# Optimization experiments

Measured on AMD Instinct MI355X. Metric: run time of the kernel, lower is better.

## Reference

```python
import jax, jax.numpy as jnp
import numpy as np


def _soft_attention(h, context, W_in, W_out):
    """Luong soft-dot attention. h: [B,H], context: [B,L,H].
    W_in: [H,H] (in,out layout), W_out: [2H,H]."""
    target = h @ W_in                                  # [B, H]
    attn = jnp.einsum('blh,bh->bl', context, target)   # [B, L]
    p = jax.nn.softmax(attn, axis=-1)                  # [B, L]
    weighted_ctx = jnp.einsum('bl,blh->bh', p, context)  # [B, H]
    h_tilde = jnp.tanh(jnp.concatenate([weighted_ctx, h], axis=1) @ W_out)  # [B, H]
    return h_tilde, p


def setup_inputs() -> dict:
    key = jax.random.key(0)
    ks = jax.random.split(key, 13)
    B, L, H = 64, 512, 1024
    s2 = 1.0 / np.sqrt(2 * H)
    s1 = 1.0 / np.sqrt(H)
    return {
        'h_tilde_s': jax.random.normal(ks[0], (B, H), jnp.float32),
        'h_tilde_o': jax.random.normal(ks[1], (B, H), jnp.float32),
        'h_tilde_a': jax.random.normal(ks[2], (B, H), jnp.float32),
        'enc_out': jax.random.normal(ks[3], (B, L, H), jnp.float32),
        'full_feature_len': 36,
        'W_as': jax.random.normal(ks[4], (2 * H, H), jnp.float32) * s2,
        'W_so': jax.random.normal(ks[5], (2 * H, H), jnp.float32) * s2,
        'W_oa': jax.random.normal(ks[6], (2 * H, H), jnp.float32) * s2,
        'Win_as': jax.random.normal(ks[7], (H, H), jnp.float32) * s1,
        'Win_so': jax.random.normal(ks[8], (H, H), jnp.float32) * s1,
        'Win_oa': jax.random.normal(ks[9], (H, H), jnp.float32) * s1,
        'Wout_as': jax.random.normal(ks[10], (2 * H, H), jnp.float32) * s2,
        'Wout_so': jax.random.normal(ks[11], (2 * H, H), jnp.float32) * s2,
        'Wout_oa': jax.random.normal(ks[12], (2 * H, H), jnp.float32) * s2,
    }


def reference(h_tilde_s, h_tilde_o, h_tilde_a, enc_out, full_feature_len,
              W_as, W_so, W_oa, Win_as, Win_so, Win_oa,
              Wout_as, Wout_so, Wout_oa):
    # Relational contexts via concat + linear(no bias) + tanh
    h_as = jnp.tanh(jnp.concatenate([h_tilde_a, h_tilde_s], axis=1) @ W_as)  # [B,H]
    h_so = jnp.tanh(jnp.concatenate([h_tilde_s, h_tilde_o], axis=1) @ W_so)
    h_oa = jnp.tanh(jnp.concatenate([h_tilde_o, h_tilde_a], axis=1) @ W_oa)
    # Three parallel soft-dot attentions over encoder output
    sa_as, _ = _soft_attention(h_as, enc_out, Win_as, Wout_as)
    sa_so, _ = _soft_attention(h_so, enc_out, Win_so, Wout_so)
    sa_oa, _ = _soft_attention(h_oa, enc_out, Win_oa, Wout_oa)
    B, H = sa_as.shape
    F = full_feature_len
    # repeat_interleave of size-1 dim == broadcast tile to [B, F, H]
    ctx_mas = jnp.broadcast_to(sa_as[:, None, :], (B, F, H))
    ctx_mso = jnp.broadcast_to(sa_so[:, None, :], (B, F, H))
    ctx_moa = jnp.broadcast_to(sa_oa[:, None, :], (B, F, H))
    return (ctx_mas, ctx_mso, ctx_moa)
```

## Files before the change

kernel.cpp:

```cpp
#include <hip/hip_runtime.h>
#include <hip/hip_cooperative_groups.h>

namespace cg = cooperative_groups;

constexpr int BB = 64;
constexpr int LL = 512;
constexpr int HH = 1024;
constexpr int SPLITS = 16;
constexpr int GRID  = 512;
constexpr int NTHR  = 256;
constexpr int NWORK_GEMM = 3 * 16 * SPLITS;

typedef float nt_float4 __attribute__((ext_vector_type(4)));

struct Args {
    const float* hs; const float* ho; const float* ha; const float* enc;
    const int* Fp;
    const float* W_as;  const float* W_so;  const float* W_oa;
    const float* Win_as; const float* Win_so; const float* Win_oa;
    const float* Wout_as; const float* Wout_so; const float* Wout_oa;
    float* part; float* hx; float* tt; float* wc; float* opm; float* ms;
    float* out;
};

template<int K0, int K1>
__device__ __forceinline__ void gemm_tile(const float* __restrict__ a0,
                                          const float* __restrict__ a1,
                                          const float* __restrict__ w,
                                          float* __restrict__ part_r,
                                          int nt, int sp, int tid,
                                          float (*As)[64], float (*Ws)[64])
{
    constexpr int K = K0 + K1;
    constexpr int KRANGE = K / SPLITS;
    const int n0 = nt << 6;
    const int ks = sp * KRANGE;
    const int tn = tid & 15;
    const int tm = tid >> 4;

    float acc[4][4] = {};

    for (int kt = ks; kt < ks + KRANGE; kt += 32) {
        {
            const int m   = tid >> 2;
            const int kk0 = (tid & 3) << 3;
            const int kg  = kt + kk0;
            const float* src = (K1 == 0 || kg < K0) ? (a0 + (size_t)m * HH + kg)
                                                    : (a1 + (size_t)m * HH + (kg - K0));
            float4 v0 = *(const float4*)(src);
            float4 v1 = *(const float4*)(src + 4);
            As[kk0 + 0][m] = v0.x; As[kk0 + 1][m] = v0.y;
            As[kk0 + 2][m] = v0.z; As[kk0 + 3][m] = v0.w;
            As[kk0 + 4][m] = v1.x; As[kk0 + 5][m] = v1.y;
            As[kk0 + 6][m] = v1.z; As[kk0 + 7][m] = v1.w;
        }
        {
            const int j4 = (tid & 15) << 2;
            int kk = tid >> 4;
            #pragma unroll
            for (int i = 0; i < 2; i++, kk += 16) {
                *(float4*)&Ws[kk][j4] = *(const float4*)(w + (size_t)(kt + kk) * HH + n0 + j4);
            }
        }
        __syncthreads();
        #pragma unroll
        for (int kk = 0; kk < 32; kk++) {
            float4 a4 = *(const float4*)&As[kk][tm << 2];
            float4 b4 = *(const float4*)&Ws[kk][tn << 2];
            float av[4] = {a4.x, a4.y, a4.z, a4.w};
            float bv[4] = {b4.x, b4.y, b4.z, b4.w};
            #pragma unroll
            for (int i = 0; i < 4; i++)
                #pragma unroll
                for (int j = 0; j < 4; j++)
                    acc[i][j] += av[i] * bv[j];
        }
        __syncthreads();
    }

    float* dst = part_r + (size_t)(sp << 6) * HH + n0 + (tn << 2);
    #pragma unroll
    for (int i = 0; i < 4; i++) {
        const int m = (tm << 2) + i;
        *(float4*)(dst + (size_t)m * HH) = make_float4(acc[i][0], acc[i][1], acc[i][2], acc[i][3]);
    }
}

__device__ __forceinline__ void gemmA_work(const Args& a, int wk, int tid,
                                           float (*As)[64], float (*Ws)[64])
{
    const int r  = wk >> 8;
    const int nt = wk & 15;
    const int sp = (wk >> 4) & 15;
    const float* a0 = (r == 0) ? a.ha : (r == 1) ? a.hs : a.ho;
    const float* a1 = (r == 0) ? a.hs : (r == 1) ? a.ho : a.ha;
    const float* w  = (r == 0) ? a.W_as : (r == 1) ? a.W_so : a.W_oa;
    gemm_tile<1024, 1024>(a0, a1, w, a.part + (size_t)r * SPLITS * 65536,
                          nt, sp, tid, As, Ws);
}

__device__ __forceinline__ void gemmC_work(const Args& a, int wk, int tid,
                                           float (*As)[64], float (*Ws)[64])
{
    const int r  = wk >> 8;
    const int nt = wk & 15;
    const int sp = (wk >> 4) & 15;
    const float* a0 = a.hx + (size_t)r * 65536;
    const float* w  = (r == 0) ? a.Win_as : (r == 1) ? a.Win_so : a.Win_oa;
    gemm_tile<1024, 0>(a0, nullptr, w, a.part + (size_t)r * SPLITS * 65536,
                       nt, sp, tid, As, Ws);
}

__device__ __forceinline__ void gemmG_work(const Args& a, int wk, int tid,
                                           float (*As)[64], float (*Ws)[64])
{
    const int r  = wk >> 8;
    const int nt = wk & 15;
    const int sp = (wk >> 4) & 15;
    const float* a0 = a.wc + (size_t)r * 65536;
    const float* a1 = a.hx + (size_t)r * 65536;
    const float* w  = (r == 0) ? a.Wout_as : (r == 1) ? a.Wout_so : a.Wout_oa;
    gemm_tile<1024, 1024>(a0, a1, w, a.part + (size_t)r * SPLITS * 65536,
                          nt, sp, tid, As, Ws);
}

__device__ __forceinline__ void reduce_phase(const float* __restrict__ part,
                                             float* __restrict__ dst,
                                             int gtid, bool do_tanh)
{
    if (gtid >= 49152) return;
    const int flat = gtid << 2;
    const int r    = flat >> 16;
    const int mn   = flat & 65535;
    const float* p = part + (size_t)r * SPLITS * 65536 + mn;
    float4 s = *(const float4*)p;
    #pragma unroll
    for (int y = 1; y < SPLITS; y++) {
        float4 q = *(const float4*)(p + (size_t)y * 65536);
        s.x += q.x; s.y += q.y; s.z += q.z; s.w += q.w;
    }
    if (do_tanh) {
        s.x = tanhf(s.x); s.y = tanhf(s.y); s.z = tanhf(s.z); s.w = tanhf(s.w);
    }
    *(float4*)(dst + (size_t)r * 65536 + mn) = s;
}

__device__ __forceinline__ void flash_phase(const Args& args, int chunk, int tid,
                                            float* smem)
{
    float (*o_l)[HH]     = (float(*)[HH])smem;
    float (*ms_sh)[3][2] = (float(*)[3][2])(smem + 4096);
    const int b    = chunk >> 3;
    const int lc   = chunk & 7;
    const int lane = tid & 63;
    const int wv   = tid >> 6;

    float4 tr[3][4];
    #pragma unroll
    for (int r = 0; r < 3; r++)
        #pragma unroll
        for (int v = 0; v < 4; v++)
            tr[r][v] = *(const float4*)&args.tt[(size_t)(r * BB + b) * HH + (lane << 2) + (v << 8)];

    float  m_run[3] = {-3.0e38f, -3.0e38f, -3.0e38f};
    float  S_run[3] = {0.f, 0.f, 0.f};
    float4 o_run[3][4];
    #pragma unroll
    for (int r = 0; r < 3; r++)
        #pragma unroll
        for (int v = 0; v < 4; v++)
            o_run[r][v] = make_float4(0.f, 0.f, 0.f, 0.f);

    const float* ebase = args.enc + ((size_t)b * LL + (lc << 6) + (wv << 2)) * HH + (lane << 2);

    for (int it = 0; it < 4; it++) {
        const float* e = ebase + (size_t)(it << 4) * HH;
        float4 ev[4][4];
        #pragma unroll
        for (int j = 0; j < 4; j++)
            #pragma unroll
            for (int v = 0; v < 4; v++)
                ev[j][v] = *(const float4*)(e + (size_t)j * HH + (v << 8));

        float s[3][4];
        #pragma unroll
        for (int j = 0; j < 4; j++) {
            float d0 = 0.f, d1 = 0.f, d2 = 0.f;
            #pragma unroll
            for (int v = 0; v < 4; v++) {
                const float4 x = ev[j][v];
                d0 += x.x * tr[0][v].x + x.y * tr[0][v].y + x.z * tr[0][v].z + x.w * tr[0][v].w;
                d1 += x.x * tr[1][v].x + x.y * tr[1][v].y + x.z * tr[1][v].z + x.w * tr[1][v].w;
                d2 += x.x * tr[2][v].x + x.y * tr[2][v].y + x.z * tr[2][v].z + x.w * tr[2][v].w;
            }
            #pragma unroll
            for (int off = 32; off > 0; off >>= 1) {
                d0 += __shfl_xor(d0, off);
                d1 += __shfl_xor(d1, off);
                d2 += __shfl_xor(d2, off);
            }
            s[0][j] = d0; s[1][j] = d1; s[2][j] = d2;
        }

        #pragma unroll
        for (int r = 0; r < 3; r++) {
            const float mb = fmaxf(fmaxf(s[r][0], s[r][1]), fmaxf(s[r][2], s[r][3]));
            const float mn_ = fmaxf(m_run[r], mb);
            const float alpha = __expf(m_run[r] - mn_);
            m_run[r] = mn_;
            float p[4];
            float psum = 0.f;
            #pragma unroll
            for (int j = 0; j < 4; j++) { p[j] = __expf(s[r][j] - mn_); psum += p[j]; }
            S_run[r] = S_run[r] * alpha + psum;
            #pragma unroll
            for (int v = 0; v < 4; v++) {
                float4 o = o_run[r][v];
                o.x *= alpha; o.y *= alpha; o.z *= alpha; o.w *= alpha;
                #pragma unroll
                for (int j = 0; j < 4; j++) {
                    const float4 x = ev[j][v];
                    o.x += p[j] * x.x; o.y += p[j] * x.y;
                    o.z += p[j] * x.z; o.w += p[j] * x.w;
                }
                o_run[r][v] = o;
            }
        }
    }

    if (lane == 0) {
        #pragma unroll
        for (int r = 0; r < 3; r++) { ms_sh[wv][r][0] = m_run[r]; ms_sh[wv][r][1] = S_run[r]; }
    }

    #pragma unroll
    for (int r = 0; r < 3; r++) {
        __syncthreads();
        #pragma unroll
        for (int v = 0; v < 4; v++)
            *(float4*)&o_l[wv][(lane << 2) + (v << 8)] = o_run[r][v];
        __syncthreads();

        const float m0 = ms_sh[0][r][0], m1 = ms_sh[1][r][0];
        const float m2 = ms_sh[2][r][0], m3 = ms_sh[3][r][0];
        const float M = fmaxf(fmaxf(m0, m1), fmaxf(m2, m3));
        const float w0 = __expf(m0 - M), w1 = __expf(m1 - M);
        const float w2 = __expf(m2 - M), w3 = __expf(m3 - M);
        float4 q0 = *(const float4*)&o_l[0][tid << 2];
        float4 q1 = *(const float4*)&o_l[1][tid << 2];
        float4 q2 = *(const float4*)&o_l[2][tid << 2];
        float4 q3 = *(const float4*)&o_l[3][tid << 2];
        float4 acc;
        acc.x = w0 * q0.x + w1 * q1.x + w2 * q2.x + w3 * q3.x;
        acc.y = w0 * q0.y + w1 * q1.y + w2 * q2.y + w3 * q3.y;
        acc.z = w0 * q0.z + w1 * q1.z + w2 * q2.z + w3 * q3.z;
        acc.w = w0 * q0.w + w1 * q1.w + w2 * q2.w + w3 * q3.w;
        *(float4*)&args.opm[((size_t)chunk * 3 + r) * HH + (tid << 2)] = acc;
        if (tid == 0) {
            const float S = w0 * ms_sh[0][r][1] + w1 * ms_sh[1][r][1]
                          + w2 * ms_sh[2][r][1] + w3 * ms_sh[3][r][1];
            args.ms[((size_t)chunk * 3 + r) * 2 + 0] = M;
            args.ms[((size_t)chunk * 3 + r) * 2 + 1] = S;
        }
    }
}

__device__ __forceinline__ void combine_phase(const Args& args, int b, int r, int tid)
{
    float mv[8], sv[8];
    float M = -3.0e38f;
    #pragma unroll
    for (int c = 0; c < 8; c++) {
        const int chunk = (b << 3) + c;
        mv[c] = args.ms[((size_t)chunk * 3 + r) * 2 + 0];
        sv[c] = args.ms[((size_t)chunk * 3 + r) * 2 + 1];
        M = fmaxf(M, mv[c]);
    }
    float S = 0.f;
    float4 acc = make_float4(0.f, 0.f, 0.f, 0.f);
    #pragma unroll
    for (int c = 0; c < 8; c++) {
        const float wgt = __expf(mv[c] - M);
        S += wgt * sv[c];
        const int chunk = (b << 3) + c;
        float4 q = *(const float4*)&args.opm[((size_t)chunk * 3 + r) * HH + (tid << 2)];
        acc.x += wgt * q.x; acc.y += wgt * q.y;
        acc.z += wgt * q.z; acc.w += wgt * q.w;
    }
    const float inv = 1.0f / S;
    acc.x *= inv; acc.y *= inv; acc.z *= inv; acc.w *= inv;
    *(float4*)&args.wc[(size_t)(r * BB + b) * HH + (tid << 2)] = acc;
}

__device__ __forceinline__ void broadcast_phase(const Args& args, int gtid)
{
    const int flat = gtid << 2;
    const int r    = flat >> 16;
    const int mn   = flat & 65535;
    const float* p = args.part + (size_t)r * SPLITS * 65536 + mn;
    float4 s = *(const float4*)p;
    #pragma unroll
    for (int y = 1; y < SPLITS; y++) {
        float4 q = *(const float4*)(p + (size_t)y * 65536);
        s.x += q.x; s.y += q.y; s.z += q.z; s.w += q.w;
    }
    s.x = tanhf(s.x); s.y = tanhf(s.y); s.z = tanhf(s.z); s.w = tanhf(s.w);

    nt_float4 sv;
    sv.x = s.x; sv.y = s.y; sv.z = s.z; sv.w = s.w;

    const int F  = *args.Fp;
    const int bb = mn >> 10;
    const int hh = mn & 1023;
    float* o = args.out + ((size_t)(r * BB + bb) * F) * HH + hh;
    for (int f = 0; f < F; f++)
        __builtin_nontemporal_store(sv, (nt_float4*)(o + (size_t)f * HH));
}

__global__ __launch_bounds__(NTHR, 2)
void mega_kernel(Args args)
{
    __shared__ __align__(16) float smem[4224];
    cg::grid_group grid = cg::this_grid();
    const int bid  = blockIdx.x;
    const int tid  = threadIdx.x;
    const int gtid = bid * NTHR + tid;

    float (*As)[64] = (float(*)[64])smem;
    float (*Ws)[64] = (float(*)[64])(smem + 2048);

    for (int wk = bid; wk < NWORK_GEMM; wk += gridDim.x)
        gemmA_work(args, wk, tid, As, Ws);
    grid.sync();

    reduce_phase(args.part, args.hx, gtid, true);
    grid.sync();

    for (int wk = bid; wk < NWORK_GEMM; wk += gridDim.x)
        gemmC_work(args, wk, tid, As, Ws);
    grid.sync();

    reduce_phase(args.part, args.tt, gtid, false);
    grid.sync();

    flash_phase(args, bid, tid, smem);
    grid.sync();

    if (bid < 192)
        combine_phase(args, bid & 63, bid >> 6, tid);
    grid.sync();

    for (int wk = bid; wk < NWORK_GEMM; wk += gridDim.x)
        gemmG_work(args, wk, tid, As, Ws);
    grid.sync();

    if (gtid < 49152)
        broadcast_phase(args, gtid);
}

__global__ __launch_bounds__(NTHR)
void k_gemmA(Args a)
{
    __shared__ __align__(16) float smem[4096];
    gemmA_work(a, blockIdx.x, threadIdx.x, (float(*)[64])smem, (float(*)[64])(smem + 2048));
}

__global__ __launch_bounds__(NTHR)
void k_gemmC(Args a)
{
    __shared__ __align__(16) float smem[4096];
    gemmC_work(a, blockIdx.x, threadIdx.x, (float(*)[64])smem, (float(*)[64])(smem + 2048));
}

__global__ __launch_bounds__(NTHR)
void k_gemmG(Args a)
{
    __shared__ __align__(16) float smem[4096];
    gemmG_work(a, blockIdx.x, threadIdx.x, (float(*)[64])smem, (float(*)[64])(smem + 2048));
}

__global__ __launch_bounds__(NTHR)
void k_reduceB(Args a) { reduce_phase(a.part, a.hx, blockIdx.x * NTHR + threadIdx.x, true); }

__global__ __launch_bounds__(NTHR)
void k_reduceD(Args a) { reduce_phase(a.part, a.tt, blockIdx.x * NTHR + threadIdx.x, false); }

__global__ __launch_bounds__(NTHR)
void k_flash(Args a)
{
    __shared__ __align__(16) float smem[4224];
    flash_phase(a, blockIdx.x, threadIdx.x, smem);
}

__global__ __launch_bounds__(NTHR)
void k_combine(Args a) { combine_phase(a, blockIdx.x, blockIdx.y, threadIdx.x); }

__global__ __launch_bounds__(NTHR)
void k_broadcast(Args a)
{
    const int gtid = blockIdx.x * NTHR + threadIdx.x;
    if (gtid < 49152) broadcast_phase(a, gtid);
}

extern "C" void kernel_launch(void* const* d_in, const int* in_sizes, int n_in,
                              void* d_out, int out_size, void* d_ws, size_t ws_size,
                              hipStream_t stream)
{
    (void)in_sizes; (void)n_in; (void)out_size; (void)ws_size;
    float* ws = (float*)d_ws;

    Args a;
    a.hs  = (const float*)d_in[0];
    a.ho  = (const float*)d_in[1];
    a.ha  = (const float*)d_in[2];
    a.enc = (const float*)d_in[3];
    a.Fp  = (const int*)d_in[4];
    a.W_as    = (const float*)d_in[5];
    a.W_so    = (const float*)d_in[6];
    a.W_oa    = (const float*)d_in[7];
    a.Win_as  = (const float*)d_in[8];
    a.Win_so  = (const float*)d_in[9];
    a.Win_oa  = (const float*)d_in[10];
    a.Wout_as = (const float*)d_in[11];
    a.Wout_so = (const float*)d_in[12];
    a.Wout_oa = (const float*)d_in[13];

    a.part = ws;
    a.hx   = ws + 3145728;
    a.tt   = ws + 3342336;
    a.wc   = ws + 3538944;
    a.opm  = ws + 3735552;
    a.ms   = ws + 5308416;
    a.out  = (float*)d_out;

    static int coop = -2;
    if (coop == -2) {
        int dev = 0, cus = 0, nb = 0;
        hipGetDevice(&dev);
        hipDeviceGetAttribute(&cus, hipDeviceAttributeMultiprocessorCount, dev);
        hipError_t e = hipOccupancyMaxActiveBlocksPerMultiprocessor(&nb, mega_kernel, NTHR, 0);
        coop = (e == hipSuccess && nb > 0 && (long)nb * cus >= GRID) ? 1 : 0;
    }

    bool launched = false;
    if (coop == 1) {
        void* kargs[] = { (void*)&a };
        hipError_t e = hipLaunchCooperativeKernel((const void*)mega_kernel,
                                                  dim3(GRID), dim3(NTHR),
                                                  kargs, 0, stream);
        launched = (e == hipSuccess);
        if (!launched) coop = 0;
    }

    if (!launched) {
        k_gemmA<<<NWORK_GEMM, NTHR, 0, stream>>>(a);
        k_reduceB<<<192, NTHR, 0, stream>>>(a);
        k_gemmC<<<NWORK_GEMM, NTHR, 0, stream>>>(a);
        k_reduceD<<<192, NTHR, 0, stream>>>(a);
        k_flash<<<512, NTHR, 0, stream>>>(a);
        k_combine<<<dim3(64, 3), NTHR, 0, stream>>>(a);
        k_gemmG<<<NWORK_GEMM, NTHR, 0, stream>>>(a);
        k_broadcast<<<192, NTHR, 0, stream>>>(a);
    }
}
```

Measured before the change: 327.4 us.

## Size cooperative grid to occupancy, split flash chunks finer, prefetch GEMM tiles

Lets the cooperative mega-kernel grid scale to occupancy (up to 1024 blocks, launch bounds raised to 4 blocks per CU) and converts every phase to grid-stride loops. The flash-attention phase is split into 1024 chunks of 32 rows each, so combine merges 16 partials per batch row; the opm/ms workspace offsets are adjusted to fit. The GEMM tile loop now register-prefetches the next A/W slice while computing the current one. Together these aim to fill more CUs and hide global latency, at the cost of more register pressure and more combine work.

Result: slower. 822.0 us (+151.1%).

```diff
diff --git a/kernel.cpp b/kernel.cpp
--- a/kernel.cpp
+++ b/kernel.cpp
@@ -7,9 +7,11 @@
 constexpr int LL = 512;
 constexpr int HH = 1024;
 constexpr int SPLITS = 16;
-constexpr int GRID  = 512;
 constexpr int NTHR  = 256;
+constexpr int MAXGRID = 1024;
 constexpr int NWORK_GEMM = 3 * 16 * SPLITS;
+constexpr int CHUNKS = 1024;
+constexpr int NWORK_RED = 49152;
 
 typedef float nt_float4 __attribute__((ext_vector_type(4)));
 
@@ -37,32 +39,44 @@
     const int ks = sp * KRANGE;
     const int tn = tid & 15;
     const int tm = tid >> 4;
+    const int m   = tid >> 2;
+    const int kk0 = (tid & 3) << 3;
+    const int j4  = (tid & 15) << 2;
+    const int kkw = tid >> 4;
+
+    float4 av0, av1, wv0, wv1;
+    {
+        const int kg = ks + kk0;
+        const float* srcA = (K1 == 0 || kg < K0) ? (a0 + (size_t)m * HH + kg)
+                                                 : (a1 + (size_t)m * HH + (kg - K0));
+        av0 = *(const float4*)srcA;
+        av1 = *(const float4*)(srcA + 4);
+        wv0 = *(const float4*)(w + (size_t)(ks + kkw) * HH + n0 + j4);
+        wv1 = *(const float4*)(w + (size_t)(ks + kkw + 16) * HH + n0 + j4);
+    }
 
     float acc[4][4] = {};
 
     for (int kt = ks; kt < ks + KRANGE; kt += 32) {
-        {
-            const int m   = tid >> 2;
-            const int kk0 = (tid & 3) << 3;
-            const int kg  = kt + kk0;
-            const float* src = (K1 == 0 || kg < K0) ? (a0 + (size_t)m * HH + kg)
-                                                    : (a1 + (size_t)m * HH + (kg - K0));
-            float4 v0 = *(const float4*)(src);
-            float4 v1 = *(const float4*)(src + 4);
-            As[kk0 + 0][m] = v0.x; As[kk0 + 1][m] = v0.y;
-            As[kk0 + 2][m] = v0.z; As[kk0 + 3][m] = v0.w;
-            As[kk0 + 4][m] = v1.x; As[kk0 + 5][m] = v1.y;
-            As[kk0 + 6][m] = v1.z; As[kk0 + 7][m] = v1.w;
+        As[kk0 + 0][m] = av0.x; As[kk0 + 1][m] = av0.y;
+        As[kk0 + 2][m] = av0.z; As[kk0 + 3][m] = av0.w;
+        As[kk0 + 4][m] = av1.x; As[kk0 + 5][m] = av1.y;
+        As[kk0 + 6][m] = av1.z; As[kk0 + 7][m] = av1.w;
+        *(float4*)&Ws[kkw][j4]      = wv0;
+        *(float4*)&Ws[kkw + 16][j4] = wv1;
+        __syncthreads();
+
+        if (kt + 32 < ks + KRANGE) {
+            const int kn = kt + 32;
+            const int kg = kn + kk0;
+            const float* srcA = (K1 == 0 || kg < K0) ? (a0 + (size_t)m * HH + kg)
+                                                     : (a1 + (size_t)m * HH + (kg - K0));
+            av0 = *(const float4*)srcA;
+            av1 = *(const float4*)(srcA + 4);
+            wv0 = *(const float4*)(w + (size_t)(kn + kkw) * HH + n0 + j4);
+            wv1 = *(const float4*)(w + (size_t)(kn + kkw + 16) * HH + n0 + j4);
         }
-        {
-            const int j4 = (tid & 15) << 2;
-            int kk = tid >> 4;
-            #pragma unroll
-            for (int i = 0; i < 2; i++, kk += 16) {
-                *(float4*)&Ws[kk][j4] = *(const float4*)(w + (size_t)(kt + kk) * HH + n0 + j4);
-            }
-        }
-        __syncthreads();
+
         #pragma unroll
         for (int kk = 0; kk < 32; kk++) {
             float4 a4 = *(const float4*)&As[kk][tm << 2];
@@ -81,8 +95,8 @@
     float* dst = part_r + (size_t)(sp << 6) * HH + n0 + (tn << 2);
     #pragma unroll
     for (int i = 0; i < 4; i++) {
-        const int m = (tm << 2) + i;
-        *(float4*)(dst + (size_t)m * HH) = make_float4(acc[i][0], acc[i][1], acc[i][2], acc[i][3]);
+        const int mm = (tm << 2) + i;
+        *(float4*)(dst + (size_t)mm * HH) = make_float4(acc[i][0], acc[i][1], acc[i][2], acc[i][3]);
     }
 }
 
@@ -124,12 +138,11 @@
                           nt, sp, tid, As, Ws);
 }
 
-__device__ __forceinline__ void reduce_phase(const float* __restrict__ part,
-                                             float* __restrict__ dst,
-                                             int gtid, bool do_tanh)
-{
-    if (gtid >= 49152) return;
-    const int flat = gtid << 2;
+__device__ __forceinline__ void reduce_slot(const float* __restrict__ part,
+                                            float* __restrict__ dst,
+                                            int slot, bool do_tanh)
+{
+    const int flat = slot << 2;
     const int r    = flat >> 16;
     const int mn   = flat & 65535;
     const float* p = part + (size_t)r * SPLITS * 65536 + mn;
@@ -150,8 +163,8 @@
 {
     float (*o_l)[HH]     = (float(*)[HH])smem;
     float (*ms_sh)[3][2] = (float(*)[3][2])(smem + 4096);
-    const int b    = chunk >> 3;
-    const int lc   = chunk & 7;
+    const int b    = chunk >> 4;
+    const int lc   = chunk & 15;
     const int lane = tid & 63;
     const int wv   = tid >> 6;
 
@@ -171,9 +184,9 @@
         for (int v = 0; v < 4; v++)
             o_run[r][v] = make_float4(0.f, 0.f, 0.f, 0.f);
 
-    const float* ebase = args.enc + ((size_t)b * LL + (lc << 6) + (wv << 2)) * HH + (lane << 2);
-
-    for (int it = 0; it < 4; it++) {
+    const float* ebase = args.enc + ((size_t)b * LL + (lc << 5) + (wv << 2)) * HH + (lane << 2);
+
+    for (int it = 0; it < 2; it++) {
         const float* e = ebase + (size_t)(it << 4) * HH;
         float4 ev[4][4];
         #pragma unroll
@@ -228,6 +241,7 @@
         }
     }
 
+    __syncthreads();
     if (lane == 0) {
         #pragma unroll
         for (int r = 0; r < 3; r++) { ms_sh[wv][r][0] = m_run[r]; ms_sh[wv][r][1] = S_run[r]; }
@@ -267,11 +281,11 @@
 
 __device__ __forceinline__ void combine_phase(const Args& args, int b, int r, int tid)
 {
-    float mv[8], sv[8];
+    float mv[16], sv[16];
     float M = -3.0e38f;
     #pragma unroll
-    for (int c = 0; c < 8; c++) {
-        const int chunk = (b << 3) + c;
+    for (int c = 0; c < 16; c++) {
+        const int chunk = (b << 4) + c;
         mv[c] = args.ms[((size_t)chunk * 3 + r) * 2 + 0];
         sv[c] = args.ms[((size_t)chunk * 3 + r) * 2 + 1];
         M = fmaxf(M, mv[c]);
@@ -279,10 +293,10 @@
     float S = 0.f;
     float4 acc = make_float4(0.f, 0.f, 0.f, 0.f);
     #pragma unroll
-    for (int c = 0; c < 8; c++) {
+    for (int c = 0; c < 16; c++) {
         const float wgt = __expf(mv[c] - M);
         S += wgt * sv[c];
-        const int chunk = (b << 3) + c;
+        const int chunk = (b << 4) + c;
         float4 q = *(const float4*)&args.opm[((size_t)chunk * 3 + r) * HH + (tid << 2)];
         acc.x += wgt * q.x; acc.y += wgt * q.y;
         acc.z += wgt * q.z; acc.w += wgt * q.w;
@@ -292,9 +306,9 @@
     *(float4*)&args.wc[(size_t)(r * BB + b) * HH + (tid << 2)] = acc;
 }
 
-__device__ __forceinline__ void broadcast_phase(const Args& args, int gtid)
-{
-    const int flat = gtid << 2;
+__device__ __forceinline__ void broadcast_slot(const Args& args, int slot)
+{
+    const int flat = slot << 2;
     const int r    = flat >> 16;
     const int mn   = flat & 65535;
     const float* p = args.part + (size_t)r * SPLITS * 65536 + mn;
@@ -317,7 +331,7 @@
         __builtin_nontemporal_store(sv, (nt_float4*)(o + (size_t)f * HH));
 }
 
-__global__ __launch_bounds__(NTHR, 2)
+__global__ __launch_bounds__(NTHR, 4)
 void mega_kernel(Args args)
 {
     __shared__ __align__(16) float smem[4224];
@@ -325,6 +339,7 @@
     const int bid  = blockIdx.x;
     const int tid  = threadIdx.x;
     const int gtid = bid * NTHR + tid;
+    const int nthreads = gridDim.x * NTHR;
 
     float (*As)[64] = (float(*)[64])smem;
     float (*Ws)[64] = (float(*)[64])(smem + 2048);
@@ -333,29 +348,32 @@
         gemmA_work(args, wk, tid, As, Ws);
     grid.sync();
 
-    reduce_phase(args.part, args.hx, gtid, true);
+    for (int i = gtid; i < NWORK_RED; i += nthreads)
+        reduce_slot(args.part, args.hx, i, true);
     grid.sync();
 
     for (int wk = bid; wk < NWORK_GEMM; wk += gridDim.x)
         gemmC_work(args, wk, tid, As, Ws);
     grid.sync();
 
-    reduce_phase(args.part, args.tt, gtid, false);
-    grid.sync();
-
-    flash_phase(args, bid, tid, smem);
-    grid.sync();
-
-    if (bid < 192)
-        combine_phase(args, bid & 63, bid >> 6, tid);
+    for (int i = gtid; i < NWORK_RED; i += nthreads)
+        reduce_slot(args.part, args.tt, i, false);
+    grid.sync();
+
+    for (int ck = bid; ck < CHUNKS; ck += gridDim.x)
+        flash_phase(args, ck, tid, smem);
+    grid.sync();
+
+    for (int wk = bid; wk < 192; wk += gridDim.x)
+        combine_phase(args, wk & 63, wk >> 6, tid);
     grid.sync();
 
     for (int wk = bid; wk < NWORK_GEMM; wk += gridDim.x)
         gemmG_work(args, wk, tid, As, Ws);
     grid.sync();
 
-    if (gtid < 49152)
-        broadcast_phase(args, gtid);
+    for (int i = gtid; i < NWORK_RED; i += nthreads)
+        broadcast_slot(args, i);
 }
 
 __global__ __launch_bounds__(NTHR)
@@ -380,10 +398,18 @@
 }
 
 __global__ __launch_bounds__(NTHR)
-void k_reduceB(Args a) { reduce_phase(a.part, a.hx, blockIdx.x * NTHR + threadIdx.x, true); }
-
-__global__ __launch_bounds__(NTHR)
-void k_reduceD(Args a) { reduce_phase(a.part, a.tt, blockIdx.x * NTHR + threadIdx.x, false); }
+void k_reduceB(Args a)
+{
+    const int i = blockIdx.x * NTHR + threadIdx.x;
+    if (i < NWORK_RED) reduce_slot(a.part, a.hx, i, true);
+}
+
+__global__ __launch_bounds__(NTHR)
+void k_reduceD(Args a)
+{
+    const int i = blockIdx.x * NTHR + threadIdx.x;
+    if (i < NWORK_RED) reduce_slot(a.part, a.tt, i, false);
+}
 
 __global__ __launch_bounds__(NTHR)
 void k_flash(Args a)
@@ -398,8 +424,8 @@
 __global__ __launch_bounds__(NTHR)
 void k_broadcast(Args a)
 {
-    const int gtid = blockIdx.x * NTHR + threadIdx.x;
-    if (gtid < 49152) broadcast_phase(a, gtid);
+    const int i = blockIdx.x * NTHR + threadIdx.x;
+    if (i < NWORK_RED) broadcast_slot(a, i);
 }
 
 extern "C" void kernel_launch(void* const* d_in, const int* in_sizes, int n_in,
@@ -430,26 +456,27 @@
     a.tt   = ws + 3342336;
     a.wc   = ws + 3538944;
     a.opm  = ws + 3735552;
-    a.ms   = ws + 5308416;
+    a.ms   = ws + 6881280;
     a.out  = (float*)d_out;
 
-    static int coop = -2;
-    if (coop == -2) {
+    static int grid_n = -1;
+    if (grid_n < 0) {
         int dev = 0, cus = 0, nb = 0;
         hipGetDevice(&dev);
         hipDeviceGetAttribute(&cus, hipDeviceAttributeMultiprocessorCount, dev);
         hipError_t e = hipOccupancyMaxActiveBlocksPerMultiprocessor(&nb, mega_kernel, NTHR, 0);
-        coop = (e == hipSuccess && nb > 0 && (long)nb * cus >= GRID) ? 1 : 0;
+        grid_n = (e == hipSuccess && nb > 0) ? ((long)nb * cus >= MAXGRID ? MAXGRID : nb * cus)
+                                             : 0;
     }
 
     bool launched = false;
-    if (coop == 1) {
+    if (grid_n > 0) {
         void* kargs[] = { (void*)&a };
         hipError_t e = hipLaunchCooperativeKernel((const void*)mega_kernel,
-                                                  dim3(GRID), dim3(NTHR),
+                                                  dim3(grid_n), dim3(NTHR),
                                                   kargs, 0, stream);
         launched = (e == hipSuccess);
-        if (!launched) coop = 0;
+        if (!launched) grid_n = 0;
     }
 
     if (!launched) {
@@ -457,7 +484,7 @@
         k_reduceB<<<192, NTHR, 0, stream>>>(a);
         k_gemmC<<<NWORK_GEMM, NTHR, 0, stream>>>(a);
         k_reduceD<<<192, NTHR, 0, stream>>>(a);
-        k_flash<<<512, NTHR, 0, stream>>>(a);
+        k_flash<<<CHUNKS, NTHR, 0, stream>>>(a);
         k_combine<<<dim3(64, 3), NTHR, 0, stream>>>(a);
         k_gemmG<<<NWORK_GEMM, NTHR, 0, stream>>>(a);
         k_broadcast<<<192, NTHR, 0, stream>>>(a);
```
